# Kernel optimization log

Hardware: AMD Instinct MI355X
Metric: run time of the kernel (lower is better)

The kernel has to match this reference:

```python
import jax, jax.numpy as jnp
import numpy as np

B = 8192
D_IN = 1024
D_H = 1024


def setup_inputs() -> dict:
    key = jax.random.key(0)
    ks = jax.random.split(key, 15)
    s_in = 1.0 / np.sqrt(D_IN)
    s_h = 1.0 / np.sqrt(D_H)
    return {
        "x": jax.random.normal(ks[0], (B, D_IN), dtype=jnp.float32),
        "h": jax.random.normal(ks[1], (B, D_H), dtype=jnp.float32),
        "c": jax.random.normal(ks[2], (B, D_H), dtype=jnp.float32),
        "Wi": jax.random.normal(ks[3], (D_H, D_IN), dtype=jnp.float32) * s_in,
        "bi": jax.random.normal(ks[4], (D_H,), dtype=jnp.float32) * s_in,
        "Ui": jax.random.normal(ks[5], (D_H, D_H), dtype=jnp.float32) * s_h,
        "Wf": jax.random.normal(ks[6], (D_H, D_IN), dtype=jnp.float32) * s_in,
        "bf": jax.random.normal(ks[7], (D_H,), dtype=jnp.float32) * s_in,
        "Uf": jax.random.normal(ks[8], (D_H, D_H), dtype=jnp.float32) * s_h,
        "Wo": jax.random.normal(ks[9], (D_H, D_IN), dtype=jnp.float32) * s_in,
        "bo": jax.random.normal(ks[10], (D_H,), dtype=jnp.float32) * s_in,
        "Uo": jax.random.normal(ks[11], (D_H, D_H), dtype=jnp.float32) * s_h,
        "Wc": jax.random.normal(ks[12], (D_H, D_IN), dtype=jnp.float32) * s_in,
        "bc": jax.random.normal(ks[13], (D_H,), dtype=jnp.float32) * s_in,
        "Uc": jax.random.normal(ks[14], (D_H, D_H), dtype=jnp.float32) * s_h,
    }


def reference(x, h, c, Wi, bi, Ui, Wf, bf, Uf, Wo, bo, Uo, Wc, bc, Uc):
    # torch Linear: y = x @ W.T + b, W is [out, in]. Same math as the 8
    # separate Linear calls, expressed as 2 concatenated GEMMs + fused gates.
    Wx = jnp.concatenate([Wi, Wf, Wo, Wc], axis=0)       # [4H, D_in]
    Uh = jnp.concatenate([Ui, Uf, Uo, Uc], axis=0)       # [4H, H]
    b = jnp.concatenate([bi, bf, bo, bc], axis=0)        # [4H]
    gates = x @ Wx.T + h @ Uh.T + b                       # [B, 4H]
    gi, gf, go, gc = jnp.split(gates, 4, axis=-1)
    i = jax.nn.sigmoid(gi)
    f = jax.nn.sigmoid(gf)
    o = jax.nn.sigmoid(go)
    c_ = jnp.tanh(gc)
    new_c = f * c + i * c_
    new_h = o * jnp.tanh(new_c)
    return new_h, new_c
```

## Files before the change

### kernel.cpp

```cpp
#include <hip/hip_runtime.h>
#include <stdint.h>

#define B_ROWS 8192
#define DH     1024
#define KTOT   2048
#define BM     256
#define BN     256
#define BK     32
#define NT     (KTOT / BK)
#define NBUF   4

using short8 = __attribute__((ext_vector_type(8))) short;
using f32x4  = __attribute__((ext_vector_type(4))) float;

__device__ __forceinline__ short bfr(float f) {
    uint32_t u = __float_as_uint(f);
    u = (u + 0x7FFFu + ((u >> 16) & 1u)) >> 16;
    return (short)u;
}

__device__ __forceinline__ float sigm(float x) {
    x = fminf(fmaxf(x, -20.f), 20.f);
    return 1.f / (1.f + __expf(-x));
}
__device__ __forceinline__ float tanh_(float x) {
    x = fminf(fmaxf(x, -10.f), 10.f);
    float e = __expf(2.f * x);
    return (e - 1.f) / (e + 1.f);
}

__device__ __forceinline__ void gl16(const void* g, void* l) {
    __builtin_amdgcn_global_load_lds(
        (const __attribute__((address_space(1))) uint32_t*)(uintptr_t)g,
        (__attribute__((address_space(3))) uint32_t*)(uint32_t)(uintptr_t)l,
        16, 0, 0);
}

__global__ __launch_bounds__(256) void build_A(const float* __restrict__ x,
                                               const float* __restrict__ h,
                                               short* __restrict__ A) {
    int t   = blockIdx.x * 256 + threadIdx.x;
    int row = t >> 8;
    int col = (t & 255) * 8;
    const float* src = (col < 1024) ? (x + (size_t)row * 1024 + col)
                                    : (h + (size_t)row * 1024 + (col - 1024));
    float4 f0 = ((const float4*)src)[0];
    float4 f1 = ((const float4*)src)[1];
    short8 o;
    o[0] = bfr(f0.x); o[1] = bfr(f0.y); o[2] = bfr(f0.z); o[3] = bfr(f0.w);
    o[4] = bfr(f1.x); o[5] = bfr(f1.y); o[6] = bfr(f1.z); o[7] = bfr(f1.w);
    *(short8*)(A + (size_t)row * KTOT + col) = o;
}

__global__ __launch_bounds__(256) void build_W(
        const float* __restrict__ Wi, const float* __restrict__ Ui,
        const float* __restrict__ Wf, const float* __restrict__ Uf,
        const float* __restrict__ Wo, const float* __restrict__ Uo,
        const float* __restrict__ Wc, const float* __restrict__ Uc,
        short* __restrict__ Wrow) {
    int row  = blockIdx.x;
    int col  = threadIdx.x * 8;
    int n    = row >> 2;
    int gate = row & 3;
    const float* Wg = (gate == 0) ? Wi : (gate == 1) ? Wf : (gate == 2) ? Wo : Wc;
    const float* Ug = (gate == 0) ? Ui : (gate == 1) ? Uf : (gate == 2) ? Uo : Uc;
    const float* src = (col < 1024) ? (Wg + (size_t)n * 1024 + col)
                                    : (Ug + (size_t)n * 1024 + (col - 1024));
    float4 f0 = ((const float4*)src)[0];
    float4 f1 = ((const float4*)src)[1];
    short8 o;
    o[0] = bfr(f0.x); o[1] = bfr(f0.y); o[2] = bfr(f0.z); o[3] = bfr(f0.w);
    o[4] = bfr(f1.x); o[5] = bfr(f1.y); o[6] = bfr(f1.z); o[7] = bfr(f1.w);
    *(short8*)(Wrow + (size_t)row * KTOT + col) = o;
}

__global__ __launch_bounds__(512, 2) void lstm_main(
        const short* __restrict__ Amat, const short* __restrict__ Wrow,
        const float* __restrict__ bi, const float* __restrict__ bff,
        const float* __restrict__ bo, const float* __restrict__ bc,
        const float* __restrict__ cin, float* __restrict__ out) {
    __shared__ __align__(16) short Wt[NBUF][BM * BK];
    __shared__ __align__(16) short At[NBUF][BN * BK];

    const int tid  = threadIdx.x;
    const int lane = tid & 63;
    const int wid  = tid >> 6;
    const int wr   = wid >> 2;
    const int wc   = wid & 3;
    const int l15  = lane & 15, l16 = lane >> 4;

    const int bid   = blockIdx.x;
    const int swz   = (bid & 7) * 64 + (bid >> 3);
    const int mtile = swz >> 5;
    const int ntile = swz & 31;
    const int m0 = mtile * BM;
    const int n0 = ntile * BN;

    const int r0 = tid >> 2;
    const int kk = (((tid & 3) ^ ((r0 >> 1) & 3))) * 8;
    const short* pw0 = Wrow + (size_t)(m0 + r0) * KTOT + kk;
    const short* pw1 = Wrow + (size_t)(m0 + r0 + 128) * KTOT + kk;
    const short* pa0 = Amat + (size_t)(n0 + r0) * KTOT + kk;
    const short* pa1 = Amat + (size_t)(n0 + r0 + 128) * KTOT + kk;

    auto stage = [&](int tt) {
        const int bb = tt & (NBUF - 1);
        short* lw = &Wt[bb][tid * 8];
        short* la = &At[bb][tid * 8];
        gl16(pw0, lw);
        gl16(pw1, lw + 4096);
        gl16(pa0, la);
        gl16(pa1, la + 4096);
        pw0 += BK; pw1 += BK; pa0 += BK; pa1 += BK;
    };

    const int koff  = (l16 ^ ((l15 >> 1) & 3)) * 8;
    const int wbase = (wr * 128 + l15) * BK + koff;
    const int abase = (wc * 64 + l15) * BK + koff;

    f32x4 acc[8][4];
    #pragma unroll
    for (int mi = 0; mi < 8; ++mi)
        #pragma unroll
        for (int ni = 0; ni < 4; ++ni)
            acc[mi][ni] = f32x4{0.f, 0.f, 0.f, 0.f};

    stage(0); stage(1); stage(2);

    #pragma unroll 4
    for (int t = 0; t < NT; ++t) {
        if (t < NT - 2) {
            asm volatile("s_waitcnt vmcnt(8)\n\ts_barrier" ::: "memory");
        } else if (t == NT - 2) {
            asm volatile("s_waitcnt vmcnt(4)\n\ts_barrier" ::: "memory");
        } else {
            asm volatile("s_waitcnt vmcnt(0)\n\ts_barrier" ::: "memory");
        }
        if (t + 3 < NT) stage(t + 3);

        const int bb = t & (NBUF - 1);
        const short* WB = &Wt[bb][0];
        const short* AB = &At[bb][0];

        short8 wf[4], af4[4], wg[4];
        #pragma unroll
        for (int mi = 0; mi < 4; ++mi)
            wf[mi] = *(const short8*)(WB + wbase + mi * 16 * BK);
        #pragma unroll
        for (int ni = 0; ni < 4; ++ni)
            af4[ni] = *(const short8*)(AB + abase + ni * 16 * BK);

        __builtin_amdgcn_s_setprio(1);
        #pragma unroll
        for (int mi = 0; mi < 4; ++mi)
            #pragma unroll
            for (int ni = 0; ni < 4; ++ni)
                acc[mi][ni] = __builtin_amdgcn_mfma_f32_16x16x32_bf16(
                    wf[mi], af4[ni], acc[mi][ni], 0, 0, 0);
        __builtin_amdgcn_s_setprio(0);

        #pragma unroll
        for (int mi = 0; mi < 4; ++mi)
            wg[mi] = *(const short8*)(WB + wbase + (64 + mi * 16) * BK);

        __builtin_amdgcn_s_setprio(1);
        #pragma unroll
        for (int mi = 0; mi < 4; ++mi)
            #pragma unroll
            for (int ni = 0; ni < 4; ++ni)
                acc[mi + 4][ni] = __builtin_amdgcn_mfma_f32_16x16x32_bf16(
                    wg[mi], af4[ni], acc[mi + 4][ni], 0, 0, 0);
        __builtin_amdgcn_s_setprio(0);
    }

    const int hbase = (m0 >> 2) + wr * 32;
    #pragma unroll
    for (int mi = 0; mi < 8; ++mi) {
        const int hcol = hbase + mi * 4 + l16;
        const float bvi = bi[hcol];
        const float bvf = bff[hcol];
        const float bvo = bo[hcol];
        const float bvc = bc[hcol];
        #pragma unroll
        for (int ni = 0; ni < 4; ++ni) {
            const size_t brow = (size_t)(n0 + wc * 64 + ni * 16 + l15);
            const float cv = cin[brow * DH + hcol];
            const float gi = acc[mi][ni][0] + bvi;
            const float gf = acc[mi][ni][1] + bvf;
            const float go = acc[mi][ni][2] + bvo;
            const float gc = acc[mi][ni][3] + bvc;
            const float nc = sigm(gf) * cv + sigm(gi) * tanh_(gc);
            const float nh = sigm(go) * tanh_(nc);
            out[brow * DH + hcol] = nh;
            out[(size_t)B_ROWS * DH + brow * DH + hcol] = nc;
        }
    }
}

extern "C" void kernel_launch(void* const* d_in, const int* in_sizes, int n_in,
                              void* d_out, int out_size, void* d_ws, size_t ws_size,
                              hipStream_t stream) {
    (void)in_sizes; (void)n_in; (void)out_size; (void)ws_size;
    const float* x  = (const float*)d_in[0];
    const float* h  = (const float*)d_in[1];
    const float* c  = (const float*)d_in[2];
    const float* Wi = (const float*)d_in[3];
    const float* bi = (const float*)d_in[4];
    const float* Ui = (const float*)d_in[5];
    const float* Wf = (const float*)d_in[6];
    const float* bf = (const float*)d_in[7];
    const float* Uf = (const float*)d_in[8];
    const float* Wo = (const float*)d_in[9];
    const float* bo = (const float*)d_in[10];
    const float* Uo = (const float*)d_in[11];
    const float* Wc = (const float*)d_in[12];
    const float* bc = (const float*)d_in[13];
    const float* Uc = (const float*)d_in[14];
    float* out = (float*)d_out;

    short* A    = (short*)d_ws;
    short* Wrow = A + (size_t)B_ROWS * KTOT;

    hipLaunchKernelGGL(build_A, dim3(8192), dim3(256), 0, stream, x, h, A);
    hipLaunchKernelGGL(build_W, dim3(4096), dim3(256), 0, stream,
                       Wi, Ui, Wf, Uf, Wo, Uo, Wc, Uc, Wrow);
    hipLaunchKernelGGL(lstm_main, dim3(512), dim3(512), 0, stream,
                       A, Wrow, bi, bf, bo, bc, c, out);
}
```

Baseline: 364.1 us.

## Restructure GEMM k-loop into double-buffered BK=64 tiles with split half-stages

```diff
diff --git a/kernel.cpp b/kernel.cpp
--- a/kernel.cpp
+++ b/kernel.cpp
@@ -6,9 +6,8 @@
 #define KTOT   2048
 #define BM     256
 #define BN     256
-#define BK     32
+#define BK     64
 #define NT     (KTOT / BK)
-#define NBUF   4
 
 using short8 = __attribute__((ext_vector_type(8))) short;
 using f32x4  = __attribute__((ext_vector_type(4))) float;
@@ -79,8 +78,7 @@
         const float* __restrict__ bi, const float* __restrict__ bff,
         const float* __restrict__ bo, const float* __restrict__ bc,
         const float* __restrict__ cin, float* __restrict__ out) {
-    __shared__ __align__(16) short Wt[NBUF][BM * BK];
-    __shared__ __align__(16) short At[NBUF][BN * BK];
+    __shared__ __align__(16) short lds[65536];
 
     const int tid  = threadIdx.x;
     const int lane = tid & 63;
@@ -90,93 +88,127 @@
     const int l15  = lane & 15, l16 = lane >> 4;
 
     const int bid   = blockIdx.x;
-    const int swz   = (bid & 7) * 64 + (bid >> 3);
-    const int mtile = swz >> 5;
-    const int ntile = swz & 31;
+    const int swzb  = (bid & 7) * 64 + (bid >> 3);
+    const int mtile = swzb >> 5;
+    const int ntile = swzb & 31;
     const int m0 = mtile * BM;
     const int n0 = ntile * BN;
 
-    const int r0 = tid >> 2;
-    const int kk = (((tid & 3) ^ ((r0 >> 1) & 3))) * 8;
-    const short* pw0 = Wrow + (size_t)(m0 + r0) * KTOT + kk;
-    const short* pw1 = Wrow + (size_t)(m0 + r0 + 128) * KTOT + kk;
-    const short* pa0 = Amat + (size_t)(n0 + r0) * KTOT + kk;
-    const short* pa1 = Amat + (size_t)(n0 + r0 + 128) * KTOT + kk;
-
-    auto stage = [&](int tt) {
-        const int bb = tt & (NBUF - 1);
-        short* lw = &Wt[bb][tid * 8];
-        short* la = &At[bb][tid * 8];
-        gl16(pw0, lw);
-        gl16(pw1, lw + 4096);
-        gl16(pa0, la);
-        gl16(pa1, la + 4096);
-        pw0 += BK; pw1 += BK; pa0 += BK; pa1 += BK;
+    const int sr = tid >> 2;
+    const int sc = (tid & 3) ^ ((tid >> 3) & 3);
+    const short* pw0 = Wrow + (size_t)(m0 + sr)       * KTOT + sc * 8;
+    const short* pw1 = Wrow + (size_t)(m0 + sr + 128) * KTOT + sc * 8;
+    const short* pa0 = Amat + (size_t)(n0 + sr)       * KTOT + sc * 8;
+    const short* pa1 = Amat + (size_t)(n0 + sr + 128) * KTOT + sc * 8;
+
+    auto stageW = [&](int buf, int kk, int tt) {
+        short* d = lds + buf * 32768 + kk * 8192 + tid * 8;
+        gl16(pw0 + tt * BK + kk * 32, d);
+        gl16(pw1 + tt * BK + kk * 32, d + 4096);
     };
-
-    const int koff  = (l16 ^ ((l15 >> 1) & 3)) * 8;
-    const int wbase = (wr * 128 + l15) * BK + koff;
-    const int abase = (wc * 64 + l15) * BK + koff;
+    auto stageA = [&](int buf, int kk, int tt) {
+        short* d = lds + buf * 32768 + 16384 + kk * 8192 + tid * 8;
+        gl16(pa0 + tt * BK + kk * 32, d);
+        gl16(pa1 + tt * BK + kk * 32, d + 4096);
+    };
+
+    const int swz8  = (l16 ^ ((l15 >> 1) & 3)) * 8;
+    const int wbase = (wr * 128 + l15) * 32 + swz8;
+    const int abase = 16384 + (wc * 64 + l15) * 32 + swz8;
 
     f32x4 acc[8][4];
     #pragma unroll
-    for (int mi = 0; mi < 8; ++mi)
+    for (int a = 0; a < 8; ++a)
         #pragma unroll
         for (int ni = 0; ni < 4; ++ni)
-            acc[mi][ni] = f32x4{0.f, 0.f, 0.f, 0.f};
-
-    stage(0); stage(1); stage(2);
-
-    #pragma unroll 4
-    for (int t = 0; t < NT; ++t) {
-        if (t < NT - 2) {
-            asm volatile("s_waitcnt vmcnt(8)\n\ts_barrier" ::: "memory");
-        } else if (t == NT - 2) {
+            acc[a][ni] = f32x4{0.f, 0.f, 0.f, 0.f};
+
+    stageW(0, 0, 0); stageA(0, 0, 0);
+    stageW(0, 1, 0); stageA(0, 1, 0);
+
+    auto tile_body = [&](int t, int buf) {
+        const int bufn = buf ^ 1;
+        const short* Lb = lds + buf * 32768;
+        const bool more = (t + 1 < NT);
+
+        asm volatile("s_waitcnt vmcnt(4)\n\ts_barrier" ::: "memory");
+        if (more) { stageW(bufn, 0, t + 1); stageA(bufn, 0, t + 1); }
+
+        short8 wf[4], af[4];
+        #pragma unroll
+        for (int mi = 0; mi < 4; ++mi)
+            wf[mi] = *(const short8*)(Lb + wbase + mi * 512);
+        #pragma unroll
+        for (int ni = 0; ni < 4; ++ni)
+            af[ni] = *(const short8*)(Lb + abase + ni * 512);
+        __builtin_amdgcn_s_setprio(1);
+        #pragma unroll
+        for (int mi = 0; mi < 4; ++mi)
+            #pragma unroll
+            for (int ni = 0; ni < 4; ++ni)
+                acc[mi][ni] = __builtin_amdgcn_mfma_f32_16x16x32_bf16(
+                    wf[mi], af[ni], acc[mi][ni], 0, 0, 0);
+        __builtin_amdgcn_s_setprio(0);
+
+        short8 wg[4];
+        #pragma unroll
+        for (int mi = 0; mi < 4; ++mi)
+            wg[mi] = *(const short8*)(Lb + wbase + (64 * 32) + mi * 512);
+        __builtin_amdgcn_s_setprio(1);
+        #pragma unroll
+        for (int mi = 0; mi < 4; ++mi)
+            #pragma unroll
+            for (int ni = 0; ni < 4; ++ni)
+                acc[4 + mi][ni] = __builtin_amdgcn_mfma_f32_16x16x32_bf16(
+                    wg[mi], af[ni], acc[4 + mi][ni], 0, 0, 0);
+        __builtin_amdgcn_s_setprio(0);
+
+        if (more) {
             asm volatile("s_waitcnt vmcnt(4)\n\ts_barrier" ::: "memory");
+            stageW(bufn, 1, t + 1); stageA(bufn, 1, t + 1);
         } else {
             asm volatile("s_waitcnt vmcnt(0)\n\ts_barrier" ::: "memory");
         }
-        if (t + 3 < NT) stage(t + 3);
-
-        const int bb = t & (NBUF - 1);
-        const short* WB = &Wt[bb][0];
-        const short* AB = &At[bb][0];
-
-        short8 wf[4], af4[4], wg[4];
-        #pragma unroll
-        for (int mi = 0; mi < 4; ++mi)
-            wf[mi] = *(const short8*)(WB + wbase + mi * 16 * BK);
+
+        short8 wf1[4], af1[4];
+        #pragma unroll
+        for (int mi = 0; mi < 4; ++mi)
+            wf1[mi] = *(const short8*)(Lb + 8192 + wbase + mi * 512);
         #pragma unroll
         for (int ni = 0; ni < 4; ++ni)
-            af4[ni] = *(const short8*)(AB + abase + ni * 16 * BK);
-
+            af1[ni] = *(const short8*)(Lb + 8192 + abase + ni * 512);
         __builtin_amdgcn_s_setprio(1);
         #pragma unroll
         for (int mi = 0; mi < 4; ++mi)
             #pragma unroll
             for (int ni = 0; ni < 4; ++ni)
                 acc[mi][ni] = __builtin_amdgcn_mfma_f32_16x16x32_bf16(
-                    wf[mi], af4[ni], acc[mi][ni], 0, 0, 0);
-        __builtin_amdgcn_s_setprio(0);
-
-        #pragma unroll
-        for (int mi = 0; mi < 4; ++mi)
-            wg[mi] = *(const short8*)(WB + wbase + (64 + mi * 16) * BK);
-
-        __builtin_amdgcn_s_setprio(1);
-        #pragma unroll
-        for (int mi = 0; mi < 4; ++mi)
-            #pragma unroll
-            for (int ni = 0; ni < 4; ++ni)
-                acc[mi + 4][ni] = __builtin_amdgcn_mfma_f32_16x16x32_bf16(
-                    wg[mi], af4[ni], acc[mi + 4][ni], 0, 0, 0);
-        __builtin_amdgcn_s_setprio(0);
+                    wf1[mi], af1[ni], acc[mi][ni], 0, 0, 0);
+        __builtin_amdgcn_s_setprio(0);
+
+        short8 wg1[4];
+        #pragma unroll
+        for (int mi = 0; mi < 4; ++mi)
+            wg1[mi] = *(const short8*)(Lb + 8192 + wbase + (64 * 32) + mi * 512);
+        __builtin_amdgcn_s_setprio(1);
+        #pragma unroll
+        for (int mi = 0; mi < 4; ++mi)
+            #pragma unroll
+            for (int ni = 0; ni < 4; ++ni)
+                acc[4 + mi][ni] = __builtin_amdgcn_mfma_f32_16x16x32_bf16(
+                    wg1[mi], af1[ni], acc[4 + mi][ni], 0, 0, 0);
+        __builtin_amdgcn_s_setprio(0);
+    };
+
+    for (int it = 0; it < NT / 2; ++it) {
+        tile_body(2 * it, 0);
+        tile_body(2 * it + 1, 1);
     }
 
     const int hbase = (m0 >> 2) + wr * 32;
     #pragma unroll
-    for (int mi = 0; mi < 8; ++mi) {
-        const int hcol = hbase + mi * 4 + l16;
+    for (int a = 0; a < 8; ++a) {
+        const int hcol = hbase + (a >> 2) * 16 + (a & 3) * 4 + l16;
         const float bvi = bi[hcol];
         const float bvf = bff[hcol];
         const float bvo = bo[hcol];
@@ -185,10 +217,10 @@
         for (int ni = 0; ni < 4; ++ni) {
             const size_t brow = (size_t)(n0 + wc * 64 + ni * 16 + l15);
             const float cv = cin[brow * DH + hcol];
-            const float gi = acc[mi][ni][0] + bvi;
-            const float gf = acc[mi][ni][1] + bvf;
-            const float go = acc[mi][ni][2] + bvo;
-            const float gc = acc[mi][ni][3] + bvc;
+            const float gi = acc[a][ni][0] + bvi;
+            const float gf = acc[a][ni][1] + bvf;
+            const float go = acc[a][ni][2] + bvo;
+            const float gc = acc[a][ni][3] + bvc;
             const float nc = sigm(gf) * cv + sigm(gi) * tanh_(gc);
             const float nh = sigm(go) * tanh_(nc);
             out[brow * DH + hcol] = nh;
```

New measurement: 365.7 us. No clear change (+0.4%).
